# Kernel optimization log

Measured on AMD Instinct MI355X. Metric: run time of the kernel, lower is better.

Reference implementation:

```python
import jax, jax.numpy as jnp
import numpy as np

THETA = 0.02


def _low_texture_mask(tgt_img):
    # grad magnitudes averaged over channels
    gx = jnp.mean(jnp.abs(tgt_img[:, :, :, :-1] - tgt_img[:, :, :, 1:]), axis=1, keepdims=True)
    gy = jnp.mean(jnp.abs(tgt_img[:, :, :-1, :] - tgt_img[:, :, 1:, :]), axis=1, keepdims=True)
    tw = jnp.zeros_like(tgt_img[:, :1, :, :])
    tw = tw.at[:, :, :, :-1].add(gx)
    tw = tw.at[:, :, :-1, :].add(gy)
    tw = tw / 2.0
    return tw < jnp.mean(tw)  # [B,1,H,W] bool: low-texture == invalid


def _forward(pred_depth, gt_depth, tgt_img, u_rand):
    B, C, H, W = gt_depth.shape
    N = H * W
    invalid = _low_texture_mask(tgt_img).reshape(B, N)          # bool [B,N]
    valid = ~invalid
    gt = gt_depth.reshape(B, N)
    pred = pred_depth.reshape(B, N)

    # Uniform sampling among valid pixels per batch (inverse-CDF on cumsum).
    vcum = jnp.cumsum(valid.astype(jnp.int32), axis=1)          # [B,N]
    nval = vcum[:, -1:]                                         # [B,1]
    u = jnp.minimum((u_rand * nval.astype(u_rand.dtype)).astype(jnp.int32), nval - 1)
    idx = jax.vmap(lambda c, uu: jnp.searchsorted(c, uu, side='right'))(vcum, u)  # [B,N]

    gt_val = jnp.take_along_axis(gt, idx, axis=1)               # z_B ground truth
    pred_val = jnp.take_along_axis(pred, idx, axis=1)           # z_B prediction

    # Relative-depth target for (invalid pixel, sampled valid pixel) pairs
    r1 = gt / gt_val
    r2 = gt_val / gt
    target = jnp.where(r1 >= 1.0 + THETA, 1.0,
                       jnp.where(r2 > 1.0 + THETA, -1.0, 0.0))

    d = pred - pred_val                                         # z_A - z_B
    nz = invalid & (target != 0.0)
    zz = invalid & (target == 0.0)

    arg = jnp.where(nz, -target * d, 0.0)
    log_loss = jnp.sum(jnp.where(nz, jnp.log1p(jnp.exp(arg)), 0.0)) / jnp.sum(nz).astype(d.dtype)
    sq_loss = jnp.sum(jnp.where(zz, d * d, 0.0)) / jnp.sum(zz).astype(d.dtype)
    return log_loss + sq_loss


def setup_inputs() -> dict:
    key = jax.random.key(0)
    k1, k2, k3, k4 = jax.random.split(key, 4)
    B, H, W = 16, 512, 1024
    pred_depth = jax.random.normal(k1, (B, 1, H, W), dtype=jnp.float32)
    gt_depth = jax.random.uniform(k2, (B, 1, H, W), dtype=jnp.float32, minval=0.01, maxval=1.0)
    tgt_img = jax.random.uniform(k3, (B, 3, H, W), dtype=jnp.float32)
    u_rand = jax.random.uniform(k4, (B, H * W), dtype=jnp.float32)
    return {"pred_depth": pred_depth, "gt_depth": gt_depth, "tgt_img": tgt_img, "u_rand": u_rand}


def reference(pred_depth, gt_depth, tgt_img, u_rand):
    return _forward(pred_depth, gt_depth, tgt_img, u_rand)
```

## Files before the change

kernel.cpp:

```cpp
#include <hip/hip_runtime.h>
#include <hip/hip_bf16.h>
#include <math.h>

#define BB 16
#define CC 3
#define HH 512
#define WW 1024
#define NN (HH * WW)
#define BN ((size_t)BB * NN)
#define RPB 4

typedef __attribute__((ext_vector_type(4))) _Float16 half4;
typedef __attribute__((ext_vector_type(2))) _Float16 h2;
typedef __attribute__((ext_vector_type(4))) float f4;


__global__ __launch_bounds__(256) void tw_sum_kernel(const float* __restrict__ img,
                                                     double* __restrict__ sum_part,
                                                     _Float16* __restrict__ tw_out) {
    int t = threadIdx.x;
    int bid = blockIdx.x;
    int b = bid >> 7;
    int h0 = (bid & 127) * RPB;
    const float* base = img + (size_t)b * CC * NN;
    int w0 = t * 4;
    bool haveR = (w0 < WW - 4);
    size_t rb = (size_t)h0 * WW + w0;
    f4 c0 = *(const f4*)(base + rb);
    f4 c1 = *(const f4*)(base + NN + rb);
    f4 c2 = *(const f4*)(base + 2 * NN + rb);
    float e0 = haveR ? base[rb + 4] : 0.f;
    float e1 = haveR ? base[NN + rb + 4] : 0.f;
    float e2 = haveR ? base[2 * NN + rb + 4] : 0.f;
    float rowacc = 0.f;
    #pragma unroll
    for (int r = 0; r < RPB; ++r) {
        int h = h0 + r;
        bool haveD = (h < HH - 1);
        size_t db = (size_t)(h + 1) * WW + w0;
        f4 d0, d1, d2;
        float f0, f1, f2;
        if (haveD) {
            d0 = *(const f4*)(base + db);
            d1 = *(const f4*)(base + NN + db);
            d2 = *(const f4*)(base + 2 * NN + db);
            f0 = haveR ? base[db + 4] : 0.f;
            f1 = haveR ? base[NN + db + 4] : 0.f;
            f2 = haveR ? base[2 * NN + db + 4] : 0.f;
        } else {
            d0 = d1 = d2 = (f4)0.f;
            f0 = f1 = f2 = 0.f;
        }
        float a0[5] = {c0.x, c0.y, c0.z, c0.w, e0};
        float a1[5] = {c1.x, c1.y, c1.z, c1.w, e1};
        float a2[5] = {c2.x, c2.y, c2.z, c2.w, e2};
        float b0[4] = {d0.x, d0.y, d0.z, d0.w};
        float b1[4] = {d1.x, d1.y, d1.z, d1.w};
        float b2[4] = {d2.x, d2.y, d2.z, d2.w};
        float tw[4];
        #pragma unroll
        for (int j = 0; j < 4; ++j) {
            float twv = 0.f;
            if (w0 + j < WW - 1)
                twv += (fabsf(a0[j]-a0[j+1]) + fabsf(a1[j]-a1[j+1]) + fabsf(a2[j]-a2[j+1])) / 3.0f;
            if (haveD)
                twv += (fabsf(a0[j]-b0[j]) + fabsf(a1[j]-b1[j]) + fabsf(a2[j]-b2[j])) / 3.0f;
            tw[j] = twv * 0.5f;
        }
        half4 hv; hv.x = (_Float16)tw[0]; hv.y = (_Float16)tw[1];
        hv.z = (_Float16)tw[2]; hv.w = (_Float16)tw[3];
        *(half4*)(tw_out + (size_t)b * NN + (size_t)h * WW + w0) = hv;
        rowacc += (tw[0] + tw[1]) + (tw[2] + tw[3]);
        c0 = d0; c1 = d1; c2 = d2; e0 = f0; e1 = f1; e2 = f2;
    }
    double acc = (double)rowacc;
    int lane = t & 63, wid = t >> 6;
    for (int o = 32; o > 0; o >>= 1) acc += __shfl_down(acc, o);
    __shared__ double sd[4];
    if (lane == 0) sd[wid] = acc;
    __syncthreads();
    if (t == 0) atomicAdd(&sum_part[bid & 63], sd[0]+sd[1]+sd[2]+sd[3]);
}

__global__ __launch_bounds__(256) void mask_kernel(const _Float16* __restrict__ tw_in,
                                                   const double* __restrict__ sum_part,
                                                   unsigned int* __restrict__ mask,
                                                   int* __restrict__ counts) {
    __shared__ float s_mean;
    __shared__ unsigned int wds[32];
    __shared__ int sv[4];
    int t = threadIdx.x;
    if (t == 0) {
        double s = 0.0;
        for (int i = 0; i < 64; ++i) s += sum_part[i];
        s_mean = (float)(s / (double)BN);
    }
    if (t < 32) wds[t] = 0;
    __syncthreads();
    float mean = s_mean;
    size_t g0 = ((size_t)blockIdx.x * 256 + t) * 4;
    half4 hv = *(const half4*)(tw_in + g0);
    unsigned int nib = ((float)hv.x < mean ? 1u : 0u) | ((float)hv.y < mean ? 2u : 0u)
                     | ((float)hv.z < mean ? 4u : 0u) | ((float)hv.w < mean ? 8u : 0u);
    atomicOr(&wds[t >> 3], nib << ((t & 7) * 4));
    int cv = 4 - __popc(nib);
    int lane = t & 63, wid = t >> 6;
    for (int o = 32; o > 0; o >>= 1) cv += __shfl_down(cv, o);
    if (lane == 0) sv[wid] = cv;
    __syncthreads();
    if (t < 32) mask[(size_t)blockIdx.x * 32 + t] = wds[t];
    if (t == 0) atomicAdd(&counts[blockIdx.x >> 3], sv[0]+sv[1]+sv[2]+sv[3]);
}

__global__ void scan_kernel(int* __restrict__ counts, int* __restrict__ nval) {
    int lane = threadIdx.x & 63;
    int row = threadIdx.x >> 6;
    int v = counts[row * 64 + lane];
    int incl = v;
    for (int o = 1; o < 64; o <<= 1) {
        int n = __shfl_up(incl, o);
        if (lane >= o) incl += n;
    }
    counts[row * 64 + lane] = incl - v;
    if (lane == 63) nval[row] = incl;
}

__global__ __launch_bounds__(256) void scatter_kernel(const unsigned int* __restrict__ mask,
                                                      const int* __restrict__ offsets,
                                                      const float* __restrict__ gt,
                                                      const float* __restrict__ pred,
                                                      h2* __restrict__ val) {
    int cglob = blockIdx.x;
    int b  = cglob >> 6;
    int t = threadIdx.x;
    __shared__ unsigned int svb[256];
    __shared__ int swoff[256];
    __shared__ int wsum[4];
    unsigned int vb = ~mask[(size_t)cglob * 256 + t];
    svb[t] = vb;
    int cnt = __popc(vb);
    int lane = t & 63, wid = t >> 6;
    int incl = cnt;
    for (int o = 1; o < 64; o <<= 1) {
        int n = __shfl_up(incl, o);
        if (lane >= o) incl += n;
    }
    if (lane == 63) wsum[wid] = incl;
    __syncthreads();
    int woff = 0;
    for (int i = 0; i < wid; i++) woff += wsum[i];
    swoff[t] = woff + incl - cnt;
    __syncthreads();
    size_t rowb = (size_t)b << 19;
    int chunkbase = offsets[cglob];
    size_t gbase = rowb + (size_t)(cglob & 63) * 8192;
    int bit = t & 31;
    unsigned int below = (bit == 0) ? 0u : ((1u << bit) - 1u);
    #pragma unroll 4
    for (int i = 0; i < 32; ++i) {
        int e = i * 256 + t;
        unsigned int bits = svb[i * 8 + (t >> 5)];
        if ((bits >> bit) & 1u) {
            int rank = chunkbase + swoff[i * 8 + (t >> 5)] + __popc(bits & below);
            size_t src = gbase + e;
            h2 o; o.x = (_Float16)gt[src]; o.y = (_Float16)pred[src];
            val[rowb + rank] = o;
        }
    }
}

__device__ __forceinline__ float fget(const f4& v, int k) {
    switch (k) { case 0: return v.x; case 1: return v.y; case 2: return v.z; default: return v.w; }
}

__global__ __launch_bounds__(256) void loss_kernel(const float* __restrict__ pred,
                                                   const float* __restrict__ gt,
                                                   const float* __restrict__ ur,
                                                   const unsigned int* __restrict__ mask,
                                                   const h2* __restrict__ val,
                                                   const int* __restrict__ nv_arr,
                                                   double* __restrict__ acc_ls,
                                                   double* __restrict__ acc_ss,
                                                   unsigned int* __restrict__ cnt_nz,
                                                   unsigned int* __restrict__ cnt_zz) {
    int t = threadIdx.x;
    int bid = blockIdx.x;
    int b = ((bid & 7) << 1) | ((bid >> 3) & 1);
    int chunk = bid >> 4;
    size_t rowb = (size_t)b << 19;
    int n0 = (chunk << 11) + t * 8;
    size_t g0 = rowb + (size_t)n0;
    unsigned int bits =
        (__builtin_nontemporal_load(&mask[g0 >> 5]) >> ((t & 3) << 3)) & 0xFFu;
    int nv = nv_arr[b];
    float fnv = (float)nv;
    f4 U[2], G[2], P[2];
    const f4* up = (const f4*)(ur + g0);
    const f4* gp = (const f4*)(gt + g0);
    const f4* pp = (const f4*)(pred + g0);
    #pragma unroll
    for (int i = 0; i < 2; ++i) {
        U[i] = __builtin_nontemporal_load(up + i);
        G[i] = __builtin_nontemporal_load(gp + i);
        P[i] = __builtin_nontemporal_load(pp + i);
    }
    float ls = 0.f, ss = 0.f;
    int cnz = 0, czz = 0;
    #pragma unroll
    for (int j = 0; j < 8; ++j) {
        if ((bits >> j) & 1u) {
            float urv = fget(U[j >> 2], j & 3);
            int u = min((int)(urv * fnv), nv - 1);
            h2 v = val[rowb + (size_t)u];
            float vx = (float)v.x, vy = (float)v.y;
            float gc = fget(G[j >> 2], j & 3);
            float pc = fget(P[j >> 2], j & 3);
            float d = pc - vy;
            if (gc >= 1.02f * vx)      { ls += __logf(1.f + __expf(-d)); ++cnz; }
            else if (vx > 1.02f * gc)  { ls += __logf(1.f + __expf( d)); ++cnz; }
            else                       { ss += d * d; ++czz; }
        }
    }
    int lane = t & 63, wid = t >> 6;
    __shared__ double sd[4];
    __shared__ unsigned int si[4];
    double lsd = (double)ls, ssd = (double)ss;
    for (int o = 32; o > 0; o >>= 1) lsd += __shfl_down(lsd, o);
    if (lane == 0) sd[wid] = lsd;
    __syncthreads();
    if (t == 0) atomicAdd(&acc_ls[bid & 63], sd[0]+sd[1]+sd[2]+sd[3]);
    __syncthreads();
    for (int o = 32; o > 0; o >>= 1) ssd += __shfl_down(ssd, o);
    if (lane == 0) sd[wid] = ssd;
    __syncthreads();
    if (t == 0) atomicAdd(&acc_ss[bid & 63], sd[0]+sd[1]+sd[2]+sd[3]);
    __syncthreads();
    for (int o = 32; o > 0; o >>= 1) cnz += __shfl_down(cnz, o);
    if (lane == 0) si[wid] = (unsigned int)cnz;
    __syncthreads();
    if (t == 0) atomicAdd(&cnt_nz[bid & 63], si[0]+si[1]+si[2]+si[3]);
    __syncthreads();
    for (int o = 32; o > 0; o >>= 1) czz += __shfl_down(czz, o);
    if (lane == 0) si[wid] = (unsigned int)czz;
    __syncthreads();
    if (t == 0) atomicAdd(&cnt_zz[bid & 63], si[0]+si[1]+si[2]+si[3]);
}

__global__ void finalize_kernel(const double* __restrict__ acc_ls,
                                const double* __restrict__ acc_ss,
                                const unsigned int* __restrict__ cnt_nz,
                                const unsigned int* __restrict__ cnt_zz,
                                float* __restrict__ out) {
    int t = threadIdx.x;
    double l = acc_ls[t], s2 = acc_ss[t];
    unsigned int a = cnt_nz[t], c = cnt_zz[t];
    for (int o = 32; o > 0; o >>= 1) {
        l  += __shfl_down(l, o);
        s2 += __shfl_down(s2, o);
        a  += __shfl_down(a, o);
        c  += __shfl_down(c, o);
    }
    if (t == 0) out[0] = (float)(l / (double)a + s2 / (double)c);
}

extern "C" void kernel_launch(void* const* d_in, const int* in_sizes, int n_in,
                              void* d_out, int out_size, void* d_ws, size_t ws_size,
                              hipStream_t stream) {
    const float* pred = (const float*)d_in[0];
    const float* gt   = (const float*)d_in[1];
    const float* img  = (const float*)d_in[2];
    const float* ur   = (const float*)d_in[3];
    float* out = (float*)d_out;

    char* ws = (char*)d_ws;
    double*       sum_part = (double*)(ws + 0);
    double*       acc_ls   = (double*)(ws + 512);
    double*       acc_ss   = (double*)(ws + 1024);
    unsigned int* cnt_nz   = (unsigned int*)(ws + 1536);
    unsigned int* cnt_zz   = (unsigned int*)(ws + 1792);
    int*          nval     = (int*)(ws + 2048);
    int*          counts   = (int*)(ws + 4096);
    unsigned int* mask     = (unsigned int*)(ws + 8192);
    h2*           val      = (h2*)(ws + (1 << 21));
    _Float16*     tw       = (_Float16*)(ws + (1 << 21));

    (void)hipMemsetAsync(ws, 0, 8192, stream);
    tw_sum_kernel <<<2048, 256, 0, stream>>>(img, sum_part, tw);
    mask_kernel   <<<8192, 256, 0, stream>>>(tw, sum_part, mask, counts);
    scan_kernel   <<<1, 1024, 0, stream>>>(counts, nval);
    scatter_kernel<<<1024, 256, 0, stream>>>(mask, counts, gt, pred, val);
    loss_kernel   <<<4096, 256, 0, stream>>>(pred, gt, ur, mask, val, nval,
                                             acc_ls, acc_ss, cnt_nz, cnt_zz);
    finalize_kernel<<<1, 64, 0, stream>>>(acc_ls, acc_ss, cnt_nz, cnt_zz, out);
}
```

Before: 111.1 us.

## Fold scan and finalize kernels into neighbors, double rows per tw block

Removes the standalone scan kernel: per-batch valid totals are now accumulated atomically in the mask kernel, and each scatter block rebuilds its own chunk offset with a wave-level prefix scan. Removes the finalize kernel by having the last loss block, found through a completion counter, do the final reduction. The tw_sum kernel now handles 8 rows per block instead of 4, halving its grid. Together these cut two kernel launches and their serialization gaps, at the cost of extra atomics and redundant per-block scans.

```diff
diff --git a/kernel.cpp b/kernel.cpp
--- a/kernel.cpp
+++ b/kernel.cpp
@@ -8,7 +8,6 @@
 #define WW 1024
 #define NN (HH * WW)
 #define BN ((size_t)BB * NN)
-#define RPB 4
 
 typedef __attribute__((ext_vector_type(4))) _Float16 half4;
 typedef __attribute__((ext_vector_type(2))) _Float16 h2;
@@ -20,8 +19,8 @@
                                                      _Float16* __restrict__ tw_out) {
     int t = threadIdx.x;
     int bid = blockIdx.x;
-    int b = bid >> 7;
-    int h0 = (bid & 127) * RPB;
+    int b = bid >> 6;
+    int h0 = (bid & 63) * 8;
     const float* base = img + (size_t)b * CC * NN;
     int w0 = t * 4;
     bool haveR = (w0 < WW - 4);
@@ -34,7 +33,7 @@
     float e2 = haveR ? base[2 * NN + rb + 4] : 0.f;
     float rowacc = 0.f;
     #pragma unroll
-    for (int r = 0; r < RPB; ++r) {
+    for (int r = 0; r < 8; ++r) {
         int h = h0 + r;
         bool haveD = (h < HH - 1);
         size_t db = (size_t)(h + 1) * WW + w0;
@@ -85,7 +84,8 @@
 __global__ __launch_bounds__(256) void mask_kernel(const _Float16* __restrict__ tw_in,
                                                    const double* __restrict__ sum_part,
                                                    unsigned int* __restrict__ mask,
-                                                   int* __restrict__ counts) {
+                                                   int* __restrict__ counts,
+                                                   int* __restrict__ nval) {
     __shared__ float s_mean;
     __shared__ unsigned int wds[32];
     __shared__ int sv[4];
@@ -109,33 +109,35 @@
     if (lane == 0) sv[wid] = cv;
     __syncthreads();
     if (t < 32) mask[(size_t)blockIdx.x * 32 + t] = wds[t];
-    if (t == 0) atomicAdd(&counts[blockIdx.x >> 3], sv[0]+sv[1]+sv[2]+sv[3]);
-}
-
-__global__ void scan_kernel(int* __restrict__ counts, int* __restrict__ nval) {
-    int lane = threadIdx.x & 63;
-    int row = threadIdx.x >> 6;
-    int v = counts[row * 64 + lane];
-    int incl = v;
-    for (int o = 1; o < 64; o <<= 1) {
-        int n = __shfl_up(incl, o);
-        if (lane >= o) incl += n;
-    }
-    counts[row * 64 + lane] = incl - v;
-    if (lane == 63) nval[row] = incl;
+    if (t == 0) {
+        int tot = sv[0] + sv[1] + sv[2] + sv[3];
+        atomicAdd(&counts[blockIdx.x >> 3], tot);
+        atomicAdd(&nval[blockIdx.x >> 9], tot);
+    }
 }
 
 __global__ __launch_bounds__(256) void scatter_kernel(const unsigned int* __restrict__ mask,
-                                                      const int* __restrict__ offsets,
+                                                      const int* __restrict__ counts,
                                                       const float* __restrict__ gt,
                                                       const float* __restrict__ pred,
                                                       h2* __restrict__ val) {
     int cglob = blockIdx.x;
     int b  = cglob >> 6;
+    int cl = cglob & 63;
     int t = threadIdx.x;
     __shared__ unsigned int svb[256];
     __shared__ int swoff[256];
     __shared__ int wsum[4];
+    __shared__ int schunkbase;
+    if (t < 64) {
+        int v = counts[b * 64 + t];
+        int incl = v;
+        for (int o = 1; o < 64; o <<= 1) {
+            int n = __shfl_up(incl, o);
+            if (t >= o) incl += n;
+        }
+        if (t == cl) schunkbase = incl - v;
+    }
     unsigned int vb = ~mask[(size_t)cglob * 256 + t];
     svb[t] = vb;
     int cnt = __popc(vb);
@@ -152,8 +154,8 @@
     swoff[t] = woff + incl - cnt;
     __syncthreads();
     size_t rowb = (size_t)b << 19;
-    int chunkbase = offsets[cglob];
-    size_t gbase = rowb + (size_t)(cglob & 63) * 8192;
+    int chunkbase = schunkbase;
+    size_t gbase = rowb + (size_t)cl * 8192;
     int bit = t & 31;
     unsigned int below = (bit == 0) ? 0u : ((1u << bit) - 1u);
     #pragma unroll 4
@@ -182,7 +184,9 @@
                                                    double* __restrict__ acc_ls,
                                                    double* __restrict__ acc_ss,
                                                    unsigned int* __restrict__ cnt_nz,
-                                                   unsigned int* __restrict__ cnt_zz) {
+                                                   unsigned int* __restrict__ cnt_zz,
+                                                   unsigned int* __restrict__ done,
+                                                   float* __restrict__ out) {
     int t = threadIdx.x;
     int bid = blockIdx.x;
     int b = ((bid & 7) << 1) | ((bid >> 3) & 1);
@@ -243,24 +247,22 @@
     for (int o = 32; o > 0; o >>= 1) czz += __shfl_down(czz, o);
     if (lane == 0) si[wid] = (unsigned int)czz;
     __syncthreads();
-    if (t == 0) atomicAdd(&cnt_zz[bid & 63], si[0]+si[1]+si[2]+si[3]);
-}
-
-__global__ void finalize_kernel(const double* __restrict__ acc_ls,
-                                const double* __restrict__ acc_ss,
-                                const unsigned int* __restrict__ cnt_nz,
-                                const unsigned int* __restrict__ cnt_zz,
-                                float* __restrict__ out) {
-    int t = threadIdx.x;
-    double l = acc_ls[t], s2 = acc_ss[t];
-    unsigned int a = cnt_nz[t], c = cnt_zz[t];
-    for (int o = 32; o > 0; o >>= 1) {
-        l  += __shfl_down(l, o);
-        s2 += __shfl_down(s2, o);
-        a  += __shfl_down(a, o);
-        c  += __shfl_down(c, o);
-    }
-    if (t == 0) out[0] = (float)(l / (double)a + s2 / (double)c);
+    if (t == 0) {
+        atomicAdd(&cnt_zz[bid & 63], si[0]+si[1]+si[2]+si[3]);
+        __threadfence();
+        unsigned int prev = atomicAdd(done, 1u);
+        if (prev == (unsigned int)(gridDim.x - 1)) {
+            double l = 0.0, s2 = 0.0;
+            unsigned long long a = 0, c = 0;
+            for (int i = 0; i < 64; ++i) {
+                l  += __hip_atomic_load(&acc_ls[i], __ATOMIC_RELAXED, __HIP_MEMORY_SCOPE_AGENT);
+                s2 += __hip_atomic_load(&acc_ss[i], __ATOMIC_RELAXED, __HIP_MEMORY_SCOPE_AGENT);
+                a  += __hip_atomic_load(&cnt_nz[i], __ATOMIC_RELAXED, __HIP_MEMORY_SCOPE_AGENT);
+                c  += __hip_atomic_load(&cnt_zz[i], __ATOMIC_RELAXED, __HIP_MEMORY_SCOPE_AGENT);
+            }
+            out[0] = (float)(l / (double)a + s2 / (double)c);
+        }
+    }
 }
 
 extern "C" void kernel_launch(void* const* d_in, const int* in_sizes, int n_in,
@@ -279,17 +281,16 @@
     unsigned int* cnt_nz   = (unsigned int*)(ws + 1536);
     unsigned int* cnt_zz   = (unsigned int*)(ws + 1792);
     int*          nval     = (int*)(ws + 2048);
+    unsigned int* done     = (unsigned int*)(ws + 3584);
     int*          counts   = (int*)(ws + 4096);
     unsigned int* mask     = (unsigned int*)(ws + 8192);
     h2*           val      = (h2*)(ws + (1 << 21));
     _Float16*     tw       = (_Float16*)(ws + (1 << 21));
 
     (void)hipMemsetAsync(ws, 0, 8192, stream);
-    tw_sum_kernel <<<2048, 256, 0, stream>>>(img, sum_part, tw);
-    mask_kernel   <<<8192, 256, 0, stream>>>(tw, sum_part, mask, counts);
-    scan_kernel   <<<1, 1024, 0, stream>>>(counts, nval);
+    tw_sum_kernel <<<1024, 256, 0, stream>>>(img, sum_part, tw);
+    mask_kernel   <<<8192, 256, 0, stream>>>(tw, sum_part, mask, counts, nval);
     scatter_kernel<<<1024, 256, 0, stream>>>(mask, counts, gt, pred, val);
     loss_kernel   <<<4096, 256, 0, stream>>>(pred, gt, ur, mask, val, nval,
-                                             acc_ls, acc_ss, cnt_nz, cnt_zz);
-    finalize_kernel<<<1, 64, 0, stream>>>(acc_ls, acc_ss, cnt_nz, cnt_zz, out);
-}
+                                             acc_ls, acc_ss, cnt_nz, cnt_zz, done, out);
+}
```

Measured after the change: 342.9 us. 209% more time.
